# Optimization experiments

Measured on AMD Instinct MI355X. Metric: run time of the kernel, lower is better.

The kernel has to match this reference:

```python
import jax, jax.numpy as jnp
import numpy as np

NEG_INF = -1000000000.0

def setup_inputs() -> dict:
    key = jax.random.key(0)
    k1, k2, k3, k4 = jax.random.split(key, 4)
    N, F_in, F_out, H = 4096, 256, 64, 4
    x = jax.random.normal(k1, (N, F_in), dtype=jnp.float32)
    adj = jax.random.randint(k2, (N, N), 0, 2, dtype=jnp.int32)
    W = jax.random.normal(k3, (H, F_in, F_out), dtype=jnp.float32) * 0.05
    a = jax.random.normal(k4, (H, 2 * F_out, 1), dtype=jnp.float32) * 0.05
    return {"x": x, "adj": adj, "W": W, "a": a}

def reference(x, adj, W, a):
    # x: [N, F_in], adj: [N, N] int, W: [H, F_in, F_out], a: [H, 2*F_out, 1]
    H, F_in, F_out = W.shape
    N = x.shape[0]
    h = jnp.einsum('nf,hfo->hno', x, W)              # [H, N, F_out]
    a1 = a[:, :F_out, 0]                             # [H, F_out] (dot with h_i part of concat)
    a2 = a[:, F_out:, 0]                             # [H, F_out] (dot with h_j part)
    f1 = jnp.einsum('hno,ho->hn', h, a1)             # [H, N]
    f2 = jnp.einsum('hno,ho->hn', h, a2)             # [H, N]
    e = f1[:, :, None] + f2[:, None, :]              # [H, N, N] == dot(concat(h_i,h_j), a)
    e = jnp.where(e >= 0, e, 0.2 * e)                # leaky_relu, slope 0.2
    mask = (adj == 0).astype(jnp.float32) * NEG_INF  # [N, N]
    alpha = jax.nn.softmax(e + mask[None], axis=-1)  # [H, N, N]
    # dropout deterministic (training=False) -> identity
    out = jnp.einsum('hij,hjo->hio', alpha, h)       # [H, N, F_out]
    # concat=True: concat heads along feature dim
    return jnp.transpose(out, (1, 0, 2)).reshape(N, H * F_out)
```

## Files before the change

### kernel.cpp

```cpp
#include <hip/hip_runtime.h>
#include <hip/hip_bf16.h>
#include <stdint.h>

#define LOG2E 1.4426950408889634f

typedef __attribute__((ext_vector_type(4))) float f4;
typedef __attribute__((ext_vector_type(4))) int   i4;
typedef __attribute__((ext_vector_type(8))) short s8;
typedef __attribute__((ext_vector_type(4))) short s4;

#if defined(__has_builtin)
# if __has_builtin(__builtin_amdgcn_exp2f)
#  define EXP2F(x) __builtin_amdgcn_exp2f(x)
# else
#  define EXP2F(x) exp2f(x)
# endif
#else
# define EXP2F(x) exp2f(x)
#endif

static __device__ __forceinline__ uint32_t fbits(float f) {
  union { float f; uint32_t u; } c; c.f = f; return c.u;
}
static __device__ __forceinline__ uint16_t bf16_rne(float f) {
  uint32_t b = fbits(f);
  b += 0x7FFFu + ((b >> 16) & 1u);
  return (uint16_t)(b >> 16);
}
static __device__ __forceinline__ float bf2f(uint16_t u) {
  union { uint32_t u; float f; } c; c.u = ((uint32_t)u) << 16; return c.f;
}

__global__ __launch_bounds__(256) void k_prep_wt(const float* __restrict__ W,
                                                 uint16_t* __restrict__ WT) {
  int idx = (blockIdx.x * 256 + threadIdx.x) * 4;
  f4 w = *(const f4*)(W + idx);
  int h = idx >> 14;
  int k = (idx >> 6) & 255;
  int o = idx & 63;
  uint16_t* base = WT + ((h << 6) + o) * 256 + k;
  base[0]   = bf16_rne(w.x);
  base[256] = bf16_rne(w.y);
  base[512] = bf16_rne(w.z);
  base[768] = bf16_rne(w.w);
}

__global__ __launch_bounds__(256) void k_gemm_h(
    const float* __restrict__ x, const uint16_t* __restrict__ WT,
    const float* __restrict__ a,
    uint16_t* __restrict__ hT, float* __restrict__ f1, float* __restrict__ f2) {
  const int N = 4096, K = 256;
  __shared__ uint16_t xs[16][264];
  int t = threadIdx.x;
  int i0 = blockIdx.x * 16;
  {
    int r = t >> 4, c = (t & 15) << 4;
    const float* src = x + (i0 + r) * K + c;
    union { uint16_t u[16]; s8 v[2]; } tmp;
    #pragma unroll
    for (int i = 0; i < 16; i += 4) {
      f4 v = *(const f4*)(src + i);
      tmp.u[i+0] = bf16_rne(v.x); tmp.u[i+1] = bf16_rne(v.y);
      tmp.u[i+2] = bf16_rne(v.z); tmp.u[i+3] = bf16_rne(v.w);
    }
    *(s8*)&xs[r][c]     = tmp.v[0];
    *(s8*)&xs[r][c + 8] = tmp.v[1];
  }
  __syncthreads();
  int wave = t >> 6, lane = t & 63, lr = lane & 15, lc = lane >> 4;
  f4 acc[4];
  #pragma unroll
  for (int cg = 0; cg < 4; ++cg) acc[cg] = (f4){0.f, 0.f, 0.f, 0.f};
  #pragma unroll
  for (int ks = 0; ks < 8; ++ks) {
    s8 af = *(const s8*)&xs[lr][ks * 32 + lc * 8];
    #pragma unroll
    for (int cg = 0; cg < 4; ++cg) {
      s8 bf = *(const s8*)(WT + ((wave << 6) + (cg << 4) + lr) * 256 + ks * 32 + lc * 8);
      acc[cg] = __builtin_amdgcn_mfma_f32_16x16x32_bf16(af, bf, acc[cg], 0, 0, 0);
    }
  }
  float p1[4] = {0, 0, 0, 0}, p2[4] = {0, 0, 0, 0};
  #pragma unroll
  for (int cg = 0; cg < 4; ++cg) {
    float a1v = a[wave * 128 + (cg << 4) + lr];
    float a2v = a[wave * 128 + 64 + (cg << 4) + lr];
    #pragma unroll
    for (int q = 0; q < 4; ++q) {
      p1[q] = fmaf(acc[cg][q], a1v, p1[q]);
      p2[q] = fmaf(acc[cg][q], a2v, p2[q]);
    }
  }
  #pragma unroll
  for (int m = 1; m <= 8; m <<= 1) {
    #pragma unroll
    for (int q = 0; q < 4; ++q) {
      p1[q] += __shfl_xor(p1[q], m, 64);
      p2[q] += __shfl_xor(p2[q], m, 64);
    }
  }
  if (lr == 0) {
    #pragma unroll
    for (int q = 0; q < 4; ++q) {
      f1[wave * N + i0 + (lc << 2) + q] = p1[q];
      f2[wave * N + i0 + (lc << 2) + q] = p2[q];
    }
  }
  #pragma unroll
  for (int cg = 0; cg < 4; ++cg) {
    union { uint16_t u[4]; s4 v; } h4;
    #pragma unroll
    for (int q = 0; q < 4; ++q) h4.u[q] = bf16_rne(acc[cg][q]);
    *(s4*)(hT + (size_t)((wave << 6) + (cg << 4) + lr) * N + i0 + (lc << 2)) = h4.v;
  }
}

__global__ __launch_bounds__(256) void k_f2max(const float* __restrict__ f2,
                                               float* __restrict__ f2m) {
  __shared__ float red[256];
  int h = blockIdx.x, t = threadIdx.x;
  float m = -1e30f;
  for (int j = t; j < 4096; j += 256) m = fmaxf(m, f2[h * 4096 + j]);
  red[t] = m;
  __syncthreads();
  for (int s = 128; s > 0; s >>= 1) {
    if (t < s) red[t] = fmaxf(red[t], red[t + s]);
    __syncthreads();
  }
  if (t == 0) f2m[h] = red[0];
}

__global__ __launch_bounds__(256) void k_attn(
    const int* __restrict__ adj, const float* __restrict__ f1,
    const float* __restrict__ f2, const float* __restrict__ f2m,
    const uint16_t* __restrict__ hT,
    uint16_t* __restrict__ Op, float* __restrict__ lp, int NP) {
  const int N = 4096;
  __shared__ float adjf[64][68];
  int p = blockIdx.x % NP, rb = blockIdx.x / NP;
  int i0 = rb << 6;
  int jcount = N / NP, jbase = p * jcount, ntiles = jcount >> 6;
  int t = threadIdx.x, wave = t >> 6, lane = t & 63, lr = lane & 15, lc = lane >> 4;

  float fm = f2m[wave];
  float d1[4], d2[4], lsum[4] = {0, 0, 0, 0};
  #pragma unroll
  for (int g = 0; g < 4; ++g) {
    float f1v = f1[wave * N + i0 + (g << 4) + lr];
    float s = f1v + fm;
    float M = fmaxf(s, 0.2f * s);
    d1[g] = fmaf(f1v, LOG2E, -M * LOG2E);
    d2[g] = fmaf(f1v, 0.2f * LOG2E, -M * LOG2E);
  }
  f4 acc[4][4];
  #pragma unroll
  for (int g = 0; g < 4; ++g)
    #pragma unroll
    for (int cg = 0; cg < 4; ++cg) acc[g][cg] = (f4){0.f, 0.f, 0.f, 0.f};

  int str = t >> 2, stc = (t & 3) << 4;
  const int* asrc = adj + (size_t)(i0 + str) * N + jbase + stc;
  const uint16_t* hTb = hT + (size_t)((wave << 6) + lr) * N + jbase + (lc << 3);
  const float* f2b = f2 + wave * N + jbase + (lc << 3);

  i4 av[4];
  #pragma unroll
  for (int i = 0; i < 4; ++i) av[i] = *(const i4*)(asrc + 4 * i);
  asrc += 64;

  for (int tile = 0; tile < ntiles; ++tile) {
    {
      float* dst = &adjf[str][stc];
      #pragma unroll
      for (int i = 0; i < 4; ++i) {
        f4 fv;
        fv.x = (float)av[i].x; fv.y = (float)av[i].y;
        fv.z = (float)av[i].z; fv.w = (float)av[i].w;
        *(f4*)(dst + 4 * i) = fv;
      }
    }
    __syncthreads();
    if (tile + 1 < ntiles) {
      #pragma unroll
      for (int i = 0; i < 4; ++i) av[i] = *(const i4*)(asrc + 4 * i);
      asrc += 64;
    }
    #pragma unroll
    for (int ks = 0; ks < 2; ++ks) {
      f4 f2v0 = *(const f4*)(f2b + tile * 64 + ks * 32);
      f4 f2v1 = *(const f4*)(f2b + tile * 64 + ks * 32 + 4);
      s8 bf[4];
      #pragma unroll
      for (int cg = 0; cg < 4; ++cg)
        bf[cg] = *(const s8*)(hTb + (size_t)(cg << 4) * N + tile * 64 + (ks << 5));
      #pragma unroll
      for (int g = 0; g < 4; ++g) {
        const float* arow = &adjf[(g << 4) + lr][(ks << 5) + (lc << 3)];
        f4 ar0 = *(const f4*)arow;
        f4 ar1 = *(const f4*)(arow + 4);
        float pe[8];
        #pragma unroll
        for (int e = 0; e < 8; ++e) {
          float f2e = (e < 4) ? f2v0[e] : f2v1[e - 4];
          float ae  = (e < 4) ? ar0[e]  : ar1[e - 4];
          float arg = fmaxf(fmaf(f2e, LOG2E, d1[g]),
                            fmaf(f2e, 0.2f * LOG2E, d2[g]));
          float pv = EXP2F(arg) * ae;
          lsum[g] += pv;
          pe[e] = pv;
        }
        union { uint32_t u[4]; s8 v; } af;
        #pragma unroll
        for (int i = 0; i < 4; ++i)
          af.u[i] = __builtin_amdgcn_perm(fbits(pe[2 * i + 1]) + 0x8000u,
                                          fbits(pe[2 * i]) + 0x8000u,
                                          0x07060302u);
        #pragma unroll
        for (int cg = 0; cg < 4; ++cg)
          acc[g][cg] = __builtin_amdgcn_mfma_f32_16x16x32_bf16(af.v, bf[cg],
                                                               acc[g][cg], 0, 0, 0);
      }
    }
    __syncthreads();
  }
  uint16_t* ob = Op + (size_t)((p << 2) + wave) * N * 64 + (size_t)i0 * 64;
  #pragma unroll
  for (int g = 0; g < 4; ++g) {
    #pragma unroll
    for (int cg = 0; cg < 4; ++cg) {
      #pragma unroll
      for (int q = 0; q < 4; ++q)
        ob[((g << 4) + (lc << 2) + q) * 64 + (cg << 4) + lr] = bf16_rne(acc[g][cg][q]);
    }
    float v = lsum[g];
    v += __shfl_xor(v, 16, 64);
    v += __shfl_xor(v, 32, 64);
    if (lane < 16) lp[(size_t)((p << 2) + wave) * N + i0 + (g << 4) + lane] = v;
  }
}

__global__ __launch_bounds__(256) void k_combine(
    const uint16_t* __restrict__ Op, const float* __restrict__ lp,
    float* __restrict__ out, int NP) {
  int idx = blockIdx.x * 256 + threadIdx.x;
  int n = idx >> 6;
  int c4 = (idx & 63) << 2;
  int h = c4 >> 6, o = c4 & 63;
  float s0 = 0, s1 = 0, s2 = 0, s3 = 0, ls = 0;
  for (int p = 0; p < NP; ++p) {
    size_t base = (size_t)((p << 2) + h) * 4096 + n;
    s4 v = *(const s4*)(Op + base * 64 + o);
    s0 += bf2f((uint16_t)v[0]); s1 += bf2f((uint16_t)v[1]);
    s2 += bf2f((uint16_t)v[2]); s3 += bf2f((uint16_t)v[3]);
    ls += lp[base];
  }
  float inv = (ls > 0.f) ? 1.0f / ls : 0.f;
  f4 r = {s0 * inv, s1 * inv, s2 * inv, s3 * inv};
  *(f4*)(out + (size_t)n * 256 + c4) = r;
}

extern "C" void kernel_launch(void* const* d_in, const int* in_sizes, int n_in,
                              void* d_out, int out_size, void* d_ws, size_t ws_size,
                              hipStream_t stream) {
  (void)in_sizes; (void)n_in; (void)out_size;
  const float* x   = (const float*)d_in[0];
  const int*   adj = (const int*)d_in[1];
  const float* W   = (const float*)d_in[2];
  const float* a   = (const float*)d_in[3];
  float* out = (float*)d_out;
  char* ws = (char*)d_ws;

  size_t oWT = 0;
  size_t oHT = oWT + 131072;
  size_t oF1 = oHT + 2097152;
  size_t oF2 = oF1 + 65536;
  size_t oFM = oF2 + 65536;
  size_t oOP = (oFM + 16 + 255) & ~(size_t)255;

  int NP = 8;
  while (NP > 1 && oOP + (size_t)NP * (2097152 + 65536) > ws_size) NP >>= 1;
  size_t oLP = oOP + (size_t)NP * 2097152;

  uint16_t* WT  = (uint16_t*)(ws + oWT);
  uint16_t* hT  = (uint16_t*)(ws + oHT);
  float*    f1  = (float*)(ws + oF1);
  float*    f2  = (float*)(ws + oF2);
  float*    f2m = (float*)(ws + oFM);
  uint16_t* Op  = (uint16_t*)(ws + oOP);
  float*    lp  = (float*)(ws + oLP);

  k_prep_wt<<<64, 256, 0, stream>>>(W, WT);
  k_gemm_h<<<256, 256, 0, stream>>>(x, WT, a, hT, f1, f2);
  k_f2max<<<4, 256, 0, stream>>>(f2, f2m);
  k_attn<<<64 * NP, 256, 0, stream>>>(adj, f1, f2, f2m, hT, Op, lp, NP);
  k_combine<<<1024, 256, 0, stream>>>(Op, lp, out, NP);
}
```

Before: 60.29 us.

## Fuse f2 max into GEMM via atomics, read adj directly, halve attention row tile

The separate f2-max reduction kernel is removed. Each wave of the h GEMM now folds its partial maximum into a global value with an order-preserving integer atomicMax, and the prep kernel resets that value first. The attention kernel drops the LDS staging of the adjacency matrix and its barriers, reading the int adjacency directly in MFMA fragment layout and using it as a select. The row tile shrinks from 64 to 32, which doubles the grid. The combine kernel is widened to 8 elements per thread. The trade-offs are redundant global adjacency reads across the four waves (which read the same adj rows), and twice as many hT and f2 loads overall because each block now covers fewer rows.

```diff
diff --git a/kernel.cpp b/kernel.cpp
--- a/kernel.cpp
+++ b/kernel.cpp
@@ -22,17 +22,29 @@
 static __device__ __forceinline__ uint32_t fbits(float f) {
   union { float f; uint32_t u; } c; c.f = f; return c.u;
 }
+static __device__ __forceinline__ float ubits(uint32_t u) {
+  union { uint32_t u; float f; } c; c.u = u; return c.f;
+}
 static __device__ __forceinline__ uint16_t bf16_rne(float f) {
   uint32_t b = fbits(f);
   b += 0x7FFFu + ((b >> 16) & 1u);
   return (uint16_t)(b >> 16);
 }
 static __device__ __forceinline__ float bf2f(uint16_t u) {
-  union { uint32_t u; float f; } c; c.u = ((uint32_t)u) << 16; return c.f;
+  return ubits(((uint32_t)u) << 16);
+}
+static __device__ __forceinline__ uint32_t fkey(float f) {
+  uint32_t u = fbits(f);
+  return (u >> 31) ? ~u : (u | 0x80000000u);
+}
+static __device__ __forceinline__ float unkey(uint32_t k) {
+  return ubits((k & 0x80000000u) ? (k ^ 0x80000000u) : ~k);
 }
 
 __global__ __launch_bounds__(256) void k_prep_wt(const float* __restrict__ W,
-                                                 uint16_t* __restrict__ WT) {
+                                                 uint16_t* __restrict__ WT,
+                                                 uint32_t* __restrict__ f2mkey) {
+  if (blockIdx.x == 0 && threadIdx.x < 4) f2mkey[threadIdx.x] = 0u;
   int idx = (blockIdx.x * 256 + threadIdx.x) * 4;
   f4 w = *(const f4*)(W + idx);
   int h = idx >> 14;
@@ -48,7 +60,8 @@
 __global__ __launch_bounds__(256) void k_gemm_h(
     const float* __restrict__ x, const uint16_t* __restrict__ WT,
     const float* __restrict__ a,
-    uint16_t* __restrict__ hT, float* __restrict__ f1, float* __restrict__ f2) {
+    uint16_t* __restrict__ hT, float* __restrict__ f1, float* __restrict__ f2,
+    uint32_t* __restrict__ f2mkey) {
   const int N = 4096, K = 256;
   __shared__ uint16_t xs[16][264];
   int t = threadIdx.x;
@@ -106,6 +119,10 @@
       f2[wave * N + i0 + (lc << 2) + q] = p2[q];
     }
   }
+  float wm = fmaxf(fmaxf(p2[0], p2[1]), fmaxf(p2[2], p2[3]));
+  wm = fmaxf(wm, __shfl_xor(wm, 16, 64));
+  wm = fmaxf(wm, __shfl_xor(wm, 32, 64));
+  if (lane == 0) atomicMax(&f2mkey[wave], fkey(wm));
   #pragma unroll
   for (int cg = 0; cg < 4; ++cg) {
     union { uint16_t u[4]; s4 v; } h4;
@@ -115,97 +132,62 @@
   }
 }
 
-__global__ __launch_bounds__(256) void k_f2max(const float* __restrict__ f2,
-                                               float* __restrict__ f2m) {
-  __shared__ float red[256];
-  int h = blockIdx.x, t = threadIdx.x;
-  float m = -1e30f;
-  for (int j = t; j < 4096; j += 256) m = fmaxf(m, f2[h * 4096 + j]);
-  red[t] = m;
-  __syncthreads();
-  for (int s = 128; s > 0; s >>= 1) {
-    if (t < s) red[t] = fmaxf(red[t], red[t + s]);
-    __syncthreads();
-  }
-  if (t == 0) f2m[h] = red[0];
-}
-
 __global__ __launch_bounds__(256) void k_attn(
     const int* __restrict__ adj, const float* __restrict__ f1,
-    const float* __restrict__ f2, const float* __restrict__ f2m,
+    const float* __restrict__ f2, const uint32_t* __restrict__ f2mkey,
     const uint16_t* __restrict__ hT,
     uint16_t* __restrict__ Op, float* __restrict__ lp, int NP) {
   const int N = 4096;
-  __shared__ float adjf[64][68];
-  int p = blockIdx.x % NP, rb = blockIdx.x / NP;
-  int i0 = rb << 6;
+  int p = blockIdx.x % NP;
+  int rb = blockIdx.x / NP;
+  int i0 = rb << 5;
   int jcount = N / NP, jbase = p * jcount, ntiles = jcount >> 6;
   int t = threadIdx.x, wave = t >> 6, lane = t & 63, lr = lane & 15, lc = lane >> 4;
 
-  float fm = f2m[wave];
-  float d1[4], d2[4], lsum[4] = {0, 0, 0, 0};
-  #pragma unroll
-  for (int g = 0; g < 4; ++g) {
+  float fm = unkey(f2mkey[wave]);
+  float d1[2], d2[2], lsum[2] = {0.f, 0.f};
+  #pragma unroll
+  for (int g = 0; g < 2; ++g) {
     float f1v = f1[wave * N + i0 + (g << 4) + lr];
     float s = f1v + fm;
     float M = fmaxf(s, 0.2f * s);
     d1[g] = fmaf(f1v, LOG2E, -M * LOG2E);
     d2[g] = fmaf(f1v, 0.2f * LOG2E, -M * LOG2E);
   }
-  f4 acc[4][4];
-  #pragma unroll
-  for (int g = 0; g < 4; ++g)
+  f4 acc[2][4];
+  #pragma unroll
+  for (int g = 0; g < 2; ++g)
     #pragma unroll
     for (int cg = 0; cg < 4; ++cg) acc[g][cg] = (f4){0.f, 0.f, 0.f, 0.f};
 
-  int str = t >> 2, stc = (t & 3) << 4;
-  const int* asrc = adj + (size_t)(i0 + str) * N + jbase + stc;
+  const int* asrc = adj + (size_t)(i0 + lr) * N + jbase + (lc << 3);
   const uint16_t* hTb = hT + (size_t)((wave << 6) + lr) * N + jbase + (lc << 3);
   const float* f2b = f2 + wave * N + jbase + (lc << 3);
 
-  i4 av[4];
-  #pragma unroll
-  for (int i = 0; i < 4; ++i) av[i] = *(const i4*)(asrc + 4 * i);
-  asrc += 64;
-
+  #pragma unroll 2
   for (int tile = 0; tile < ntiles; ++tile) {
-    {
-      float* dst = &adjf[str][stc];
-      #pragma unroll
-      for (int i = 0; i < 4; ++i) {
-        f4 fv;
-        fv.x = (float)av[i].x; fv.y = (float)av[i].y;
-        fv.z = (float)av[i].z; fv.w = (float)av[i].w;
-        *(f4*)(dst + 4 * i) = fv;
-      }
-    }
-    __syncthreads();
-    if (tile + 1 < ntiles) {
-      #pragma unroll
-      for (int i = 0; i < 4; ++i) av[i] = *(const i4*)(asrc + 4 * i);
-      asrc += 64;
-    }
     #pragma unroll
     for (int ks = 0; ks < 2; ++ks) {
-      f4 f2v0 = *(const f4*)(f2b + tile * 64 + ks * 32);
-      f4 f2v1 = *(const f4*)(f2b + tile * 64 + ks * 32 + 4);
+      int joff = tile * 64 + (ks << 5);
+      f4 f2v0 = *(const f4*)(f2b + joff);
+      f4 f2v1 = *(const f4*)(f2b + joff + 4);
       s8 bf[4];
       #pragma unroll
       for (int cg = 0; cg < 4; ++cg)
-        bf[cg] = *(const s8*)(hTb + (size_t)(cg << 4) * N + tile * 64 + (ks << 5));
+        bf[cg] = *(const s8*)(hTb + (size_t)(cg << 4) * N + joff);
       #pragma unroll
-      for (int g = 0; g < 4; ++g) {
-        const float* arow = &adjf[(g << 4) + lr][(ks << 5) + (lc << 3)];
-        f4 ar0 = *(const f4*)arow;
-        f4 ar1 = *(const f4*)(arow + 4);
+      for (int g = 0; g < 2; ++g) {
+        const int* ap = asrc + (size_t)(g << 4) * N + joff;
+        i4 a0 = *(const i4*)ap;
+        i4 a1 = *(const i4*)(ap + 4);
         float pe[8];
         #pragma unroll
         for (int e = 0; e < 8; ++e) {
           float f2e = (e < 4) ? f2v0[e] : f2v1[e - 4];
-          float ae  = (e < 4) ? ar0[e]  : ar1[e - 4];
+          int   ai  = (e < 4) ? a0[e]   : a1[e - 4];
           float arg = fmaxf(fmaf(f2e, LOG2E, d1[g]),
                             fmaf(f2e, 0.2f * LOG2E, d2[g]));
-          float pv = EXP2F(arg) * ae;
+          float pv = ai ? EXP2F(arg) : 0.f;
           lsum[g] += pv;
           pe[e] = pv;
         }
@@ -221,11 +203,10 @@
                                                                acc[g][cg], 0, 0, 0);
       }
     }
-    __syncthreads();
   }
   uint16_t* ob = Op + (size_t)((p << 2) + wave) * N * 64 + (size_t)i0 * 64;
   #pragma unroll
-  for (int g = 0; g < 4; ++g) {
+  for (int g = 0; g < 2; ++g) {
     #pragma unroll
     for (int cg = 0; cg < 4; ++cg) {
       #pragma unroll
@@ -243,20 +224,24 @@
     const uint16_t* __restrict__ Op, const float* __restrict__ lp,
     float* __restrict__ out, int NP) {
   int idx = blockIdx.x * 256 + threadIdx.x;
-  int n = idx >> 6;
-  int c4 = (idx & 63) << 2;
-  int h = c4 >> 6, o = c4 & 63;
-  float s0 = 0, s1 = 0, s2 = 0, s3 = 0, ls = 0;
+  int n = idx >> 5;
+  int c8 = (idx & 31) << 3;
+  int h = c8 >> 6, o = c8 & 63;
+  float s[8] = {0, 0, 0, 0, 0, 0, 0, 0};
+  float ls = 0.f;
   for (int p = 0; p < NP; ++p) {
     size_t base = (size_t)((p << 2) + h) * 4096 + n;
-    s4 v = *(const s4*)(Op + base * 64 + o);
-    s0 += bf2f((uint16_t)v[0]); s1 += bf2f((uint16_t)v[1]);
-    s2 += bf2f((uint16_t)v[2]); s3 += bf2f((uint16_t)v[3]);
+    s8 v = *(const s8*)(Op + base * 64 + o);
+    #pragma unroll
+    for (int k = 0; k < 8; ++k) s[k] += bf2f((uint16_t)v[k]);
     ls += lp[base];
   }
   float inv = (ls > 0.f) ? 1.0f / ls : 0.f;
-  f4 r = {s0 * inv, s1 * inv, s2 * inv, s3 * inv};
-  *(f4*)(out + (size_t)n * 256 + c4) = r;
+  f4 r0 = {s[0] * inv, s[1] * inv, s[2] * inv, s[3] * inv};
+  f4 r1 = {s[4] * inv, s[5] * inv, s[6] * inv, s[7] * inv};
+  float* dst = out + (size_t)n * 256 + c8;
+  *(f4*)dst = r0;
+  *(f4*)(dst + 4) = r1;
 }
 
 extern "C" void kernel_launch(void* const* d_in, const int* in_sizes, int n_in,
@@ -281,17 +266,16 @@
   while (NP > 1 && oOP + (size_t)NP * (2097152 + 65536) > ws_size) NP >>= 1;
   size_t oLP = oOP + (size_t)NP * 2097152;
 
-  uint16_t* WT  = (uint16_t*)(ws + oWT);
-  uint16_t* hT  = (uint16_t*)(ws + oHT);
-  float*    f1  = (float*)(ws + oF1);
-  float*    f2  = (float*)(ws + oF2);
-  float*    f2m = (float*)(ws + oFM);
-  uint16_t* Op  = (uint16_t*)(ws + oOP);
-  float*    lp  = (float*)(ws + oLP);
-
-  k_prep_wt<<<64, 256, 0, stream>>>(W, WT);
-  k_gemm_h<<<256, 256, 0, stream>>>(x, WT, a, hT, f1, f2);
-  k_f2max<<<4, 256, 0, stream>>>(f2, f2m);
-  k_attn<<<64 * NP, 256, 0, stream>>>(adj, f1, f2, f2m, hT, Op, lp, NP);
-  k_combine<<<1024, 256, 0, stream>>>(Op, lp, out, NP);
-}
+  uint16_t* WT   = (uint16_t*)(ws + oWT);
+  uint16_t* hT   = (uint16_t*)(ws + oHT);
+  float*    f1   = (float*)(ws + oF1);
+  float*    f2   = (float*)(ws + oF2);
+  uint32_t* f2mk = (uint32_t*)(ws + oFM);
+  uint16_t* Op   = (uint16_t*)(ws + oOP);
+  float*    lp   = (float*)(ws + oLP);
+
+  k_prep_wt<<<64, 256, 0, stream>>>(W, WT, f2mk);
+  k_gemm_h<<<256, 256, 0, stream>>>(x, WT, a, hT, f1, f2, f2mk);
+  k_attn<<<128 * NP, 256, 0, stream>>>(adj, f1, f2, f2mk, hT, Op, lp, NP);
+  k_combine<<<512, 256, 0, stream>>>(Op, lp, out, NP);
+}
```

After: 99.04 us. +64.3%, slower.
